# Optimization experiments

Hardware: AMD Instinct MI355X
Metric: run time of the kernel (lower is better)

The kernel has to match this reference:

```python
import jax, jax.numpy as jnp
import numpy as np

N_SPARSE = 26
VOCAB = 50000
EMB_DIM = 64
DENSE_DIM = 13
INPUT_DIM = N_SPARSE * EMB_DIM + DENSE_DIM  # 1677
HIDDEN = [1024, 512, 256]
N_CROSS = 3
BATCH = 16384
EPS = 1e-5


def setup_inputs() -> dict:
    key = jax.random.key(0)
    ks = jax.random.split(key, 24)
    inp = {}
    inp["sparse_data"] = jax.random.randint(ks[0], (BATCH, N_SPARSE), 0, VOCAB, dtype=jnp.int64 if jax.config.jax_enable_x64 else jnp.int32)
    inp["dense_data"] = jax.random.normal(ks[1], (BATCH, DENSE_DIM), dtype=jnp.float32)
    # stacked embedding tables [F, V, E] (nn.Embedding default init N(0,1); scaled down for stability)
    inp["emb_tables"] = jax.random.normal(ks[2], (N_SPARSE, VOCAB, EMB_DIM), dtype=jnp.float32) * 0.1
    # cross layers: Linear(input_dim, 1) per layer -> weight [L, D], bias [L]
    inp["w_cross"] = jax.random.normal(ks[3], (N_CROSS, INPUT_DIM), dtype=jnp.float32) * 0.02
    inp["b_cross"] = jnp.zeros((N_CROSS,), dtype=jnp.float32)
    # deep tower
    inp["bn0_g"] = jnp.ones((INPUT_DIM,), jnp.float32); inp["bn0_b"] = jnp.zeros((INPUT_DIM,), jnp.float32)
    inp["W1"] = jax.random.normal(ks[4], (INPUT_DIM, HIDDEN[0]), jnp.float32) * 0.02
    inp["bias1"] = jnp.zeros((HIDDEN[0],), jnp.float32)
    inp["bn1_g"] = jnp.ones((HIDDEN[0],), jnp.float32); inp["bn1_b"] = jnp.zeros((HIDDEN[0],), jnp.float32)
    inp["W2"] = jax.random.normal(ks[5], (HIDDEN[0], HIDDEN[1]), jnp.float32) * 0.02
    inp["bias2"] = jnp.zeros((HIDDEN[1],), jnp.float32)
    inp["bn2_g"] = jnp.ones((HIDDEN[1],), jnp.float32); inp["bn2_b"] = jnp.zeros((HIDDEN[1],), jnp.float32)
    inp["W3"] = jax.random.normal(ks[6], (HIDDEN[1], HIDDEN[2]), jnp.float32) * 0.02
    inp["bias3"] = jnp.zeros((HIDDEN[2],), jnp.float32)
    inp["bn3_g"] = jnp.ones((HIDDEN[2],), jnp.float32); inp["bn3_b"] = jnp.zeros((HIDDEN[2],), jnp.float32)
    # predict: Linear(hidden[-1] + input_dim, 1)
    inp["Wp"] = jax.random.normal(ks[7], (HIDDEN[2] + INPUT_DIM, 1), jnp.float32) * 0.02
    inp["bp"] = jnp.zeros((1,), jnp.float32)
    return inp


def _bn(x, g, b):
    # BatchNorm1d, training mode: biased batch stats over batch dim
    mu = jnp.mean(x, axis=0)
    var = jnp.mean((x - mu) ** 2, axis=0)
    return g * (x - mu) * jax.lax.rsqrt(var + EPS) + b


def reference(sparse_data, dense_data, emb_tables, w_cross, b_cross,
              bn0_g, bn0_b, W1, bias1, bn1_g, bn1_b, W2, bias2, bn2_g, bn2_b,
              W3, bias3, bn3_g, bn3_b, Wp, bp):
    # --- embedding (faithful to source bug: column 0 is used for every feature) ---
    idx0 = sparse_data[:, 0]                         # [B]
    emb = emb_tables[:, idx0, :]                     # [F, B, E]
    emb = jnp.transpose(emb, (1, 0, 2)).reshape(idx0.shape[0], -1)  # [B, F*E]

    x0 = jnp.concatenate([emb, dense_data], axis=1)  # [B, D]

    # --- cross network: Linear_i(x0^T x0) + x0 == x0*(x0@w_i) + b_i + x0 ---
    # (source restarts from cross_input each iteration, so only last layer matters;
    #  loop kept for fidelity, it is cheap)
    cross = x0
    for i in range(N_CROSS):
        s = x0 @ w_cross[i]                          # [B]
        cross = x0 * s[:, None] + b_cross[i] + x0    # [B, D]

    # --- deep tower: BN -> (Linear -> Dropout(eval=id) -> BN) x3, no activations ---
    h = _bn(x0, bn0_g, bn0_b)
    h = _bn(h @ W1 + bias1, bn1_g, bn1_b)
    h = _bn(h @ W2 + bias2, bn2_g, bn2_b)
    h = _bn(h @ W3 + bias3, bn3_g, bn3_b)

    out = jnp.concatenate([cross, h], axis=1) @ Wp + bp  # [B, 1]
    return jax.nn.sigmoid(out)
```

## Files before the change

### kernel.cpp

```cpp
#include <hip/hip_runtime.h>
#include <hip/hip_bf16.h>
#include <cstdint>
#include <cstddef>

#define AS1 __attribute__((address_space(1)))
#define AS3 __attribute__((address_space(3)))

typedef __attribute__((ext_vector_type(8))) short short8v;
typedef __attribute__((ext_vector_type(4))) float f32x4;
typedef unsigned short u16;

constexpr int kBatch = 16384;
constexpr int kNSp   = 26;
constexpr int kVocab = 50000;
constexpr int kEmb   = 64;
constexpr int kInDim = 1677;
constexpr int kInPad = 1728;
constexpr int kDense = 13;
constexpr int kH1 = 1024, kH2 = 512, kH3 = 256;
constexpr float kEps = 1e-5f;

constexpr int kStatsFloats = 2 * (kInPad + kH1 + kH2 + kH3);
constexpr int kBfFloats    = kH1 + kH2 + kH3;

__device__ __forceinline__ float b2f(u16 s) {
  unsigned u = ((unsigned)s) << 16;
  union { unsigned u; float f; } c; c.u = u; return c.f;
}
__device__ __forceinline__ u16 f2b(float f) {
  __hip_bfloat16 h = __float2bfloat16(f);
  return __builtin_bit_cast(u16, h);
}

__global__ void gather_kernel(const int* __restrict__ sparse, const float* __restrict__ dense,
                              const float* __restrict__ emb, const float* __restrict__ w_cross,
                              const float* __restrict__ b_cross, const float* __restrict__ Wp,
                              u16* __restrict__ x0, float* __restrict__ crossc,
                              float* __restrict__ stats) {
  const int b = blockIdx.x;
  const int tid = threadIdx.x;
  if (b == 0) {
    for (int i = tid; i < kStatsFloats + kBfFloats; i += 256) stats[i] = 0.f;
  }
  const int idx = sparse[b * kNSp];
  const float* wc2 = w_cross + 2 * kInDim;
  u16* xrow = x0 + (size_t)b * kInPad;
  float u = 0.f, v = 0.f, w = 0.f;
  for (int q = tid; q < 416; q += 256) {
    int p = q * 4;
    const float* src = emb + ((size_t)(p >> 6) * kVocab + idx) * kEmb + (p & 63);
    float4 val = *(const float4*)src;
    float4 wp  = *(const float4*)(Wp + p);
    u += val.x * wc2[p] + val.y * wc2[p + 1] + val.z * wc2[p + 2] + val.w * wc2[p + 3];
    v += val.x * wp.x + val.y * wp.y + val.z * wp.z + val.w * wp.w;
    w += wp.x + wp.y + wp.z + wp.w;
    ushort4 o;
    o.x = f2b(val.x); o.y = f2b(val.y); o.z = f2b(val.z); o.w = f2b(val.w);
    *(ushort4*)(xrow + p) = o;
  }
  int p = 1664 + tid;
  if (p < kInPad) {
    float val = 0.f;
    if (p < kInDim) {
      val = dense[b * kDense + (p - 1664)];
      float wp = Wp[p];
      u += val * wc2[p];
      v += val * wp;
      w += wp;
    }
    xrow[p] = f2b(val);
  }
  #pragma unroll
  for (int off = 32; off; off >>= 1) {
    u += __shfl_down(u, off, 64);
    v += __shfl_down(v, off, 64);
    w += __shfl_down(w, off, 64);
  }
  __shared__ float su[4], sv[4], sw[4];
  int lane = tid & 63, wv = tid >> 6;
  if (lane == 0) { su[wv] = u; sv[wv] = v; sw[wv] = w; }
  __syncthreads();
  if (tid == 0) {
    float uu = su[0] + su[1] + su[2] + su[3];
    float vv = sv[0] + sv[1] + sv[2] + sv[3];
    float ww = sw[0] + sw[1] + sw[2] + sw[3];
    crossc[b] = (1.f + uu) * vv + b_cross[2] * ww;
  }
}

__global__ __launch_bounds__(256) void colstats_kernel(
    const u16* __restrict__ X, int ld, float* __restrict__ sum, float* __restrict__ sq) {
  const int tid = threadIdx.x;
  const int cg = tid & 7;
  const int rg = tid >> 3;
  const int col0 = blockIdx.x * 64 + cg * 8;
  const int r0 = blockIdx.y * 512 + rg;
  float s[8] = {0,0,0,0,0,0,0,0}, s2[8] = {0,0,0,0,0,0,0,0};
  for (int i = 0; i < 16; ++i) {
    int r = r0 + i * 32;
    short8v v = *(const short8v*)(X + (size_t)r * ld + col0);
    #pragma unroll
    for (int e = 0; e < 8; ++e) {
      float f = b2f((u16)v[e]);
      s[e] += f; s2[e] += f * f;
    }
  }
  __shared__ float sh[256][17];
  #pragma unroll
  for (int e = 0; e < 8; ++e) { sh[tid][e] = s[e]; sh[tid][e + 8] = s2[e]; }
  __syncthreads();
  if (tid < 64) {
    int cgr = tid >> 3, e = tid & 7;
    float ts = 0.f, tq = 0.f;
    #pragma unroll
    for (int g = 0; g < 32; ++g) {
      ts += sh[g * 8 + cgr][e];
      tq += sh[g * 8 + cgr][e + 8];
    }
    int col = blockIdx.x * 64 + cgr * 8 + e;
    atomicAdd(&sum[col], ts);
    atomicAdd(&sq[col],  tq);
  }
}

__global__ void fold_kernel(const float* __restrict__ W, const float* __restrict__ sum,
                            const float* __restrict__ sq, const float* __restrict__ g,
                            const float* __restrict__ bb, float invM,
                            u16* __restrict__ Wt, float* __restrict__ bfold,
                            int K, int N, int Kp) {
  __shared__ float t[64][65];
  int kb = blockIdx.x * 64;
  int nb = blockIdx.y * 64;
  int c  = threadIdx.x & 63;
  int r0 = threadIdx.x >> 6;
  #pragma unroll
  for (int rr = 0; rr < 64; rr += 4) {
    int k = kb + rr + r0;
    t[rr + r0][c] = (k < K) ? W[(size_t)k * N + nb + c] : 0.f;
  }
  __syncthreads();
  int k = kb + c;
  float a = 0.f, cc = 0.f;
  if (k < K) {
    float mu  = sum[k] * invM;
    float var = sq[k] * invM - mu * mu;
    a  = g[k] * rsqrtf(var + kEps);
    cc = bb[k] - a * mu;
  }
  #pragma unroll
  for (int rr = 0; rr < 64; rr += 4) {
    int n = nb + rr + r0;
    float w = t[c][rr + r0];
    Wt[(size_t)n * Kp + k] = f2b(w * a);
    float part = cc * w;
    #pragma unroll
    for (int off = 32; off; off >>= 1) part += __shfl_xor(part, off, 64);
    if (c == 0) atomicAdd(&bfold[n], part);
  }
}

__global__ __launch_bounds__(256) void gemm_kernel(
    const u16* __restrict__ A, const u16* __restrict__ Bt,
    const float* __restrict__ bias, const float* __restrict__ bfold,
    u16* __restrict__ Z, float* __restrict__ sum, float* __restrict__ sq,
    int M, int N, int Kp) {
  __shared__ char lds[32768];
  char* ldsA = lds;
  char* ldsB = lds + 16384;
  const int tid  = threadIdx.x;
  const int lane = tid & 63;
  const int wv   = tid >> 6;
  const int wr = wv >> 1, wc = wv & 1;
  const int r16 = lane & 15, kg = lane >> 4;

  const int L   = blockIdx.y * gridDim.x + blockIdx.x;
  const int xcd = L & 7;
  const int j   = L >> 3;
  const int mb  = xcd * 16 + (j & 15);
  const int nb  = j >> 4;
  const int m0 = mb * 128;
  const int n0 = nb * 128;
  const int ldb = Kp * 2;

  const char* gA = (const char*)A + (size_t)m0 * ldb;
  const char* gB = (const char*)Bt + (size_t)n0 * ldb;

  const char* srcA[4]; const char* srcB[4]; int dst[4];
  #pragma unroll
  for (int rr = 0; rr < 4; ++rr) {
    int lb  = (rr * 256 + tid) * 16;
    int row = lb >> 7;
    int kb  = lb & 127;
    int kbs = kb ^ ((row & 7) << 4);
    dst[rr]  = lb;
    srcA[rr] = gA + (size_t)row * ldb + kbs;
    srcB[rr] = gB + (size_t)row * ldb + kbs;
  }

  f32x4 acc[4][4];
  #pragma unroll
  for (int m = 0; m < 4; ++m)
    #pragma unroll
    for (int n = 0; n < 4; ++n) acc[m][n] = (f32x4){0.f, 0.f, 0.f, 0.f};

  for (int k0 = 0; k0 < Kp; k0 += 64) {
    __syncthreads();
    #pragma unroll
    for (int rr = 0; rr < 4; ++rr)
      __builtin_amdgcn_global_load_lds((const AS1 unsigned*)(srcA[rr] + k0 * 2),
                                       (AS3 unsigned*)(ldsA + dst[rr]), 16, 0, 0);
    #pragma unroll
    for (int rr = 0; rr < 4; ++rr)
      __builtin_amdgcn_global_load_lds((const AS1 unsigned*)(srcB[rr] + k0 * 2),
                                       (AS3 unsigned*)(ldsB + dst[rr]), 16, 0, 0);
    asm volatile("s_waitcnt vmcnt(0)" ::: "memory");
    __syncthreads();
    #pragma unroll
    for (int kk = 0; kk < 2; ++kk) {
      short8v av[4], bv[4];
      #pragma unroll
      for (int m = 0; m < 4; ++m) {
        int row = wr * 64 + m * 16 + r16;
        int kb  = (kk * 64 + kg * 16) ^ ((row & 7) << 4);
        av[m] = *(const short8v*)(ldsA + row * 128 + kb);
      }
      #pragma unroll
      for (int n = 0; n < 4; ++n) {
        int row = wc * 64 + n * 16 + r16;
        int kb  = (kk * 64 + kg * 16) ^ ((row & 7) << 4);
        bv[n] = *(const short8v*)(ldsB + row * 128 + kb);
      }
      #pragma unroll
      for (int m = 0; m < 4; ++m)
        #pragma unroll
        for (int n = 0; n < 4; ++n)
          acc[m][n] = __builtin_amdgcn_mfma_f32_16x16x32_bf16(av[m], bv[n], acc[m][n], 0, 0, 0);
    }
  }
  #pragma unroll
  for (int n = 0; n < 4; ++n) {
    int col = n0 + wc * 64 + n * 16 + r16;
    float bs = bias[col] + bfold[col];
    float ps = 0.f, pq = 0.f;
    #pragma unroll
    for (int m = 0; m < 4; ++m) {
      int rbase = m0 + wr * 64 + m * 16 + kg * 4;
      #pragma unroll
      for (int j2 = 0; j2 < 4; ++j2) {
        float val = acc[m][n][j2] + bs;
        Z[(size_t)(rbase + j2) * N + col] = f2b(val);
        ps += val; pq += val * val;
      }
    }
    ps += __shfl_xor(ps, 16, 64); ps += __shfl_xor(ps, 32, 64);
    pq += __shfl_xor(pq, 16, 64); pq += __shfl_xor(pq, 32, 64);
    if (lane < 16) {
      atomicAdd(&sum[col], ps);
      atomicAdd(&sq[col],  pq);
    }
  }
}

#define BAR_VMN(N)                                                              \
  {                                                                             \
    asm volatile("s_waitcnt vmcnt(" #N ")" ::: "memory");                       \
    __builtin_amdgcn_sched_barrier(0);                                          \
    __builtin_amdgcn_s_barrier();                                               \
    __builtin_amdgcn_sched_barrier(0);                                          \
  }
#define BAR_NOVM()                                                              \
  {                                                                             \
    __builtin_amdgcn_sched_barrier(0);                                          \
    __builtin_amdgcn_s_barrier();                                               \
    __builtin_amdgcn_sched_barrier(0);                                          \
  }

#define STAGE(OP, H, TILE)                                                      \
  {                                                                             \
    const char* sb = ((OP) ? gB : gA) + (size_t)((H) * 128) * ldb               \
                     + (size_t)(TILE) * 128 + srcoff;                           \
    char* db = lds + (((TILE) & 1) << 16) + ((OP) << 15) + ((H) << 14) + tid * 16; \
    __builtin_amdgcn_global_load_lds((const AS1 unsigned*)sb,                   \
                                     (AS3 unsigned*)db, 16, 0, 0);              \
    __builtin_amdgcn_global_load_lds((const AS1 unsigned*)(sb + 64 * (size_t)ldb), \
                                     (AS3 unsigned*)(db + 8192), 16, 0, 0);     \
  }

#define PHASE(T, MH, NH)                                                        \
  {                                                                             \
    char* la  = lds + (((T) & 1) << 16);                                        \
    char* lbp = la + 32768;                                                     \
    short8v av[4][2], bv[2][2];                                                 \
    _Pragma("unroll")                                                           \
    for (int fm = 0; fm < 4; ++fm) {                                            \
      int row = (MH) * 128 + wr * 64 + fm * 16 + r16;                           \
      _Pragma("unroll")                                                         \
      for (int kk = 0; kk < 2; ++kk) {                                          \
        int kb = (kk * 64 + kg * 16) ^ ((row & 7) << 4);                        \
        av[fm][kk] = *(const short8v*)(la + row * 128 + kb);                    \
      }                                                                         \
    }                                                                           \
    _Pragma("unroll")                                                           \
    for (int fn = 0; fn < 2; ++fn) {                                            \
      int row = (NH) * 128 + wc * 32 + fn * 16 + r16;                           \
      _Pragma("unroll")                                                         \
      for (int kk = 0; kk < 2; ++kk) {                                          \
        int kb = (kk * 64 + kg * 16) ^ ((row & 7) << 4);                        \
        bv[fn][kk] = *(const short8v*)(lbp + row * 128 + kb);                   \
      }                                                                         \
    }                                                                           \
    __builtin_amdgcn_s_setprio(1);                                              \
    _Pragma("unroll")                                                           \
    for (int fm = 0; fm < 4; ++fm)                                              \
      _Pragma("unroll")                                                         \
      for (int fn = 0; fn < 2; ++fn)                                            \
        _Pragma("unroll")                                                       \
        for (int kk = 0; kk < 2; ++kk)                                          \
          acc[(MH) * 4 + fm][(NH) * 2 + fn] =                                   \
              __builtin_amdgcn_mfma_f32_16x16x32_bf16(                          \
                  av[fm][kk], bv[fn][kk],                                       \
                  acc[(MH) * 4 + fm][(NH) * 2 + fn], 0, 0, 0);                  \
    __builtin_amdgcn_s_setprio(0);                                              \
  }

__global__ __launch_bounds__(512, 2) void gemm256_kernel(
    const u16* __restrict__ A, const u16* __restrict__ Bt,
    const float* __restrict__ bias, const float* __restrict__ bfold,
    u16* __restrict__ Z, float* __restrict__ sum, float* __restrict__ sq,
    int M, int N, int Kp) {
  __shared__ char lds[131072];
  const int tid  = threadIdx.x;
  const int lane = tid & 63;
  const int wid  = tid >> 6;
  const int wr = wid >> 2, wc = wid & 3;
  const int r16 = lane & 15, kg = lane >> 4;

  const int nmb = M >> 8;
  const int cpx = nmb >> 3;
  const int L   = blockIdx.x;
  const int xcd = L & 7;
  const int jj  = L >> 3;
  const int mb  = xcd * cpx + (jj % cpx);
  const int nb  = jj / cpx;
  const int m0  = mb * 256;
  const int n0  = nb * 256;
  const int ldb = Kp * 2;
  const int nt  = Kp >> 6;

  const char* gA = (const char*)A + (size_t)m0 * ldb;
  const char* gB = (const char*)Bt + (size_t)n0 * ldb;
  const int row0 = tid >> 3;
  const int kbs  = ((tid & 7) * 16) ^ ((row0 & 7) << 4);
  const size_t srcoff = (size_t)row0 * ldb + kbs;

  f32x4 acc[8][4];
  #pragma unroll
  for (int m = 0; m < 8; ++m)
    #pragma unroll
    for (int n = 0; n < 4; ++n) acc[m][n] = (f32x4){0.f, 0.f, 0.f, 0.f};

  STAGE(0, 0, 0); STAGE(1, 0, 0); STAGE(1, 1, 0); STAGE(0, 1, 0);
  STAGE(0, 0, 1); STAGE(1, 0, 1);
  BAR_VMN(8);

  const int Tmain = nt - 2;
  for (int T = 0; T < Tmain; ++T) {
    STAGE(1, 1, T + 1);
    PHASE(T, 0, 0);
    BAR_VMN(8);
    STAGE(0, 1, T + 1);
    PHASE(T, 0, 1);
    BAR_VMN(8);
    if (T + 2 < nt) STAGE(0, 0, T + 2);
    PHASE(T, 1, 0);
    BAR_NOVM();
    if (T + 2 < nt) STAGE(1, 0, T + 2);
    PHASE(T, 1, 1);
    BAR_VMN(8);
  }
  for (int T = Tmain; T < nt; ++T) {
    if (T + 1 < nt) STAGE(1, 1, T + 1);
    PHASE(T, 0, 0);
    BAR_VMN(0);
    if (T + 1 < nt) STAGE(0, 1, T + 1);
    PHASE(T, 0, 1);
    BAR_VMN(0);
    PHASE(T, 1, 0);
    BAR_NOVM();
    PHASE(T, 1, 1);
    BAR_VMN(0);
  }

  #pragma unroll
  for (int nh = 0; nh < 2; ++nh)
    #pragma unroll
    for (int fn = 0; fn < 2; ++fn) {
      int col = n0 + nh * 128 + wc * 32 + fn * 16 + r16;
      float bs = bias[col] + bfold[col];
      float ps = 0.f, pq = 0.f;
      #pragma unroll
      for (int mh = 0; mh < 2; ++mh)
        #pragma unroll
        for (int fm = 0; fm < 4; ++fm) {
          int rbase = m0 + mh * 128 + wr * 64 + fm * 16 + kg * 4;
          #pragma unroll
          for (int j2 = 0; j2 < 4; ++j2) {
            float val = acc[mh * 4 + fm][nh * 2 + fn][j2] + bs;
            Z[(size_t)(rbase + j2) * N + col] = f2b(val);
            ps += val; pq += val * val;
          }
        }
      ps += __shfl_xor(ps, 16, 64); ps += __shfl_xor(ps, 32, 64);
      pq += __shfl_xor(pq, 16, 64); pq += __shfl_xor(pq, 32, 64);
      if (lane < 16) {
        atomicAdd(&sum[col], ps);
        atomicAdd(&sq[col],  pq);
      }
    }
}

#define STAGE2A(H, TILE)                                                        \
  {                                                                             \
    const char* sb = gA + (size_t)((H) * 128) * ldb + (size_t)(TILE) * 128 + srcoff; \
    char* db = lds + (((TILE) & 1) << 15) + ((H) << 14) + tid * 16;             \
    __builtin_amdgcn_global_load_lds((const AS1 unsigned*)sb,                   \
                                     (AS3 unsigned*)db, 16, 0, 0);              \
    __builtin_amdgcn_global_load_lds((const AS1 unsigned*)(sb + 64 * (size_t)ldb), \
                                     (AS3 unsigned*)(db + 8192), 16, 0, 0);     \
  }
#define STAGE2B(TILE)                                                           \
  {                                                                             \
    const char* sb = gB + (size_t)(TILE) * 128 + srcoff;                        \
    char* db = lds + 65536 + (((TILE) & 1) << 14) + tid * 16;                   \
    __builtin_amdgcn_global_load_lds((const AS1 unsigned*)sb,                   \
                                     (AS3 unsigned*)db, 16, 0, 0);              \
    __builtin_amdgcn_global_load_lds((const AS1 unsigned*)(sb + 64 * (size_t)ldb), \
                                     (AS3 unsigned*)(db + 8192), 16, 0, 0);     \
  }

#define PHASE2(T, MH)                                                           \
  {                                                                             \
    char* la  = lds + (((T) & 1) << 15) + ((MH) << 14);                         \
    char* lbp = lds + 65536 + (((T) & 1) << 14);                                \
    short8v av[4][2], bv[2][2];                                                 \
    _Pragma("unroll")                                                           \
    for (int fm = 0; fm < 4; ++fm) {                                            \
      int row = wr * 64 + fm * 16 + r16;                                        \
      _Pragma("unroll")                                                         \
      for (int kk = 0; kk < 2; ++kk) {                                          \
        int kb = (kk * 64 + kg * 16) ^ ((row & 7) << 4);                        \
        av[fm][kk] = *(const short8v*)(la + row * 128 + kb);                    \
      }                                                                         \
    }                                                                           \
    _Pragma("unroll")                                                           \
    for (int fn = 0; fn < 2; ++fn) {                                            \
      int row = wc * 32 + fn * 16 + r16;                                        \
      _Pragma("unroll")                                                         \
      for (int kk = 0; kk < 2; ++kk) {                                          \
        int kb = (kk * 64 + kg * 16) ^ ((row & 7) << 4);                        \
        bv[fn][kk] = *(const short8v*)(lbp + row * 128 + kb);                   \
      }                                                                         \
    }                                                                           \
    __builtin_amdgcn_s_setprio(1);                                              \
    _Pragma("unroll")                                                           \
    for (int fm = 0; fm < 4; ++fm)                                              \
      _Pragma("unroll")                                                         \
      for (int fn = 0; fn < 2; ++fn)                                            \
        _Pragma("unroll")                                                       \
        for (int kk = 0; kk < 2; ++kk)                                          \
          acc[(MH) * 4 + fm][fn] =                                              \
              __builtin_amdgcn_mfma_f32_16x16x32_bf16(                          \
                  av[fm][kk], bv[fn][kk], acc[(MH) * 4 + fm][fn], 0, 0, 0);     \
    __builtin_amdgcn_s_setprio(0);                                              \
  }

__global__ __launch_bounds__(512, 2) void gemm256x128_kernel(
    const u16* __restrict__ A, const u16* __restrict__ Bt,
    const float* __restrict__ bias, const float* __restrict__ bfold,
    u16* __restrict__ Z, float* __restrict__ sum, float* __restrict__ sq,
    int M, int N, int Kp) {
  __shared__ char lds[98304];
  const int tid  = threadIdx.x;
  const int lane = tid & 63;
  const int wid  = tid >> 6;
  const int wr = wid >> 2, wc = wid & 3;
  const int r16 = lane & 15, kg = lane >> 4;

  const int nmb = M >> 8;
  const int cpx = nmb >> 3;
  const int L   = blockIdx.x;
  const int xcd = L & 7;
  const int jj  = L >> 3;
  const int mb  = xcd * cpx + (jj % cpx);
  const int nb  = jj / cpx;
  const int m0  = mb * 256;
  const int n0  = nb * 128;
  const int ldb = Kp * 2;
  const int nt  = Kp >> 6;

  const char* gA = (const char*)A + (size_t)m0 * ldb;
  const char* gB = (const char*)Bt + (size_t)n0 * ldb;
  const int row0 = tid >> 3;
  const int kbs  = ((tid & 7) * 16) ^ ((row0 & 7) << 4);
  const size_t srcoff = (size_t)row0 * ldb + kbs;

  f32x4 acc[8][2];
  #pragma unroll
  for (int m = 0; m < 8; ++m)
    #pragma unroll
    for (int n = 0; n < 2; ++n) acc[m][n] = (f32x4){0.f, 0.f, 0.f, 0.f};

  STAGE2A(0, 0); STAGE2B(0); STAGE2A(1, 0);

  const int Tmain = nt - 1;
  for (int T = 0; T < Tmain; ++T) {
    STAGE2A(0, T + 1); STAGE2B(T + 1);
    BAR_VMN(6);
    PHASE2(T, 0);
    STAGE2A(1, T + 1);
    BAR_VMN(6);
    PHASE2(T, 1);
    BAR_NOVM();
  }
  BAR_VMN(2);
  PHASE2(nt - 1, 0);
  BAR_VMN(0);
  PHASE2(nt - 1, 1);

  #pragma unroll
  for (int fn = 0; fn < 2; ++fn) {
    int col = n0 + wc * 32 + fn * 16 + r16;
    float bs = bias[col] + bfold[col];
    float ps = 0.f, pq = 0.f;
    #pragma unroll
    for (int mh = 0; mh < 2; ++mh)
      #pragma unroll
      for (int fm = 0; fm < 4; ++fm) {
        int rbase = m0 + mh * 128 + wr * 64 + fm * 16 + kg * 4;
        #pragma unroll
        for (int j2 = 0; j2 < 4; ++j2) {
          float val = acc[mh * 4 + fm][fn][j2] + bs;
          Z[(size_t)(rbase + j2) * N + col] = f2b(val);
          ps += val; pq += val * val;
        }
      }
    ps += __shfl_xor(ps, 16, 64); ps += __shfl_xor(ps, 32, 64);
    pq += __shfl_xor(pq, 16, 64); pq += __shfl_xor(pq, 32, 64);
    if (lane < 16) {
      atomicAdd(&sum[col], ps);
      atomicAdd(&sq[col],  pq);
    }
  }
}

__global__ void final_kernel(const u16* __restrict__ z3, const float* __restrict__ sum3,
                             const float* __restrict__ sq3, const float* __restrict__ g3,
                             const float* __restrict__ b3, float invM,
                             const float* __restrict__ Wp, const float* __restrict__ bp,
                             const float* __restrict__ crossc, float* __restrict__ out) {
  int wv = threadIdx.x >> 6, lane = threadIdx.x & 63;
  int b = blockIdx.x * 4 + wv;
  const float* wph = Wp + kInDim;
  float s = 0.f;
  #pragma unroll
  for (int k = lane; k < kH3; k += 64) {
    float mu  = sum3[k] * invM;
    float var = sq3[k] * invM - mu * mu;
    float a   = g3[k] * rsqrtf(var + kEps);
    float cc  = b3[k] - a * mu;
    float h = a * b2f(z3[(size_t)b * kH3 + k]) + cc;
    s += h * wph[k];
  }
  #pragma unroll
  for (int off = 32; off; off >>= 1) s += __shfl_down(s, off, 64);
  if (lane == 0) {
    float logit = s + crossc[b] + bp[0];
    out[b] = 1.f / (1.f + expf(-logit));
  }
}

constexpr size_t OFF_X0    = 0;
constexpr size_t OFF_Z1    = OFF_X0 + (size_t)kBatch * kInPad * 2;
constexpr size_t OFF_Z2    = OFF_Z1 + (size_t)kBatch * kH1 * 2;
constexpr size_t OFF_Z3    = OFF_Z2 + (size_t)kBatch * kH2 * 2;
constexpr size_t OFF_W1T   = OFF_Z3 + (size_t)kBatch * kH3 * 2;
constexpr size_t OFF_W2T   = OFF_W1T + (size_t)kH1 * kInPad * 2;
constexpr size_t OFF_W3T   = OFF_W2T + (size_t)kH2 * kH1 * 2;
constexpr size_t OFF_CROSS = OFF_W3T + (size_t)kH3 * kH2 * 2;
constexpr size_t OFF_STATS = OFF_CROSS + (size_t)kBatch * 4;
constexpr size_t OFF_BF    = OFF_STATS + (size_t)kStatsFloats * 4;

extern "C" void kernel_launch(void* const* d_in, const int* in_sizes, int n_in,
                              void* d_out, int out_size, void* d_ws, size_t ws_size,
                              hipStream_t stream) {
  const int*   sparse  = (const int*)d_in[0];
  const float* dense   = (const float*)d_in[1];
  const float* emb     = (const float*)d_in[2];
  const float* w_cross = (const float*)d_in[3];
  const float* b_cross = (const float*)d_in[4];
  const float* bn0_g = (const float*)d_in[5],  *bn0_b = (const float*)d_in[6];
  const float* W1    = (const float*)d_in[7],  *bias1 = (const float*)d_in[8];
  const float* bn1_g = (const float*)d_in[9],  *bn1_b = (const float*)d_in[10];
  const float* W2    = (const float*)d_in[11], *bias2 = (const float*)d_in[12];
  const float* bn2_g = (const float*)d_in[13], *bn2_b = (const float*)d_in[14];
  const float* W3    = (const float*)d_in[15], *bias3 = (const float*)d_in[16];
  const float* bn3_g = (const float*)d_in[17], *bn3_b = (const float*)d_in[18];
  const float* Wp    = (const float*)d_in[19], *bp    = (const float*)d_in[20];

  char* ws = (char*)d_ws;
  u16* x0  = (u16*)(ws + OFF_X0);
  u16* z1  = (u16*)(ws + OFF_Z1);
  u16* z2  = (u16*)(ws + OFF_Z2);
  u16* z3  = (u16*)(ws + OFF_Z3);
  u16* W1t = (u16*)(ws + OFF_W1T);
  u16* W2t = (u16*)(ws + OFF_W2T);
  u16* W3t = (u16*)(ws + OFF_W3T);
  float* crossc = (float*)(ws + OFF_CROSS);
  float* stats  = (float*)(ws + OFF_STATS);
  float* sum0 = stats,            *sq0 = stats + kInPad;
  float* sum1 = sq0 + kInPad,     *sq1 = sum1 + kH1;
  float* sum2 = sq1 + kH1,        *sq2 = sum2 + kH2;
  float* sum3 = sq2 + kH2,        *sq3 = sum3 + kH3;
  float* bfold = (float*)(ws + OFF_BF);
  float* b1f = bfold, *b2f = b1f + kH1, *b3f = b2f + kH2;
  float* out = (float*)d_out;

  const float invM = 1.f / (float)kBatch;

  gather_kernel<<<kBatch, 256, 0, stream>>>(sparse, dense, emb, w_cross, b_cross, Wp,
                                            x0, crossc, stats);

  colstats_kernel<<<dim3(kInPad / 64, kBatch / 512), 256, 0, stream>>>(x0, kInPad, sum0, sq0);
  fold_kernel<<<dim3(kInPad / 64, kH1 / 64), 256, 0, stream>>>(
      W1, sum0, sq0, bn0_g, bn0_b, invM, W1t, b1f, kInDim, kH1, kInPad);

  gemm256_kernel<<<(kBatch / 256) * (kH1 / 256), 512, 0, stream>>>(
      x0, W1t, bias1, b1f, z1, sum1, sq1, kBatch, kH1, kInPad);
  fold_kernel<<<dim3(kH1 / 64, kH2 / 64), 256, 0, stream>>>(
      W2, sum1, sq1, bn1_g, bn1_b, invM, W2t, b2f, kH1, kH2, kH1);

  gemm256x128_kernel<<<(kBatch / 256) * (kH2 / 128), 512, 0, stream>>>(
      z1, W2t, bias2, b2f, z2, sum2, sq2, kBatch, kH2, kH1);
  fold_kernel<<<dim3(kH2 / 64, kH3 / 64), 256, 0, stream>>>(
      W3, sum2, sq2, bn2_g, bn2_b, invM, W3t, b3f, kH2, kH3, kH2);

  gemm_kernel<<<dim3(kH3 / 128, kBatch / 128), 256, 0, stream>>>(
      z2, W3t, bias3, b3f, z3, sum3, sq3, kBatch, kH3, kH2);

  final_kernel<<<kBatch / 4, 256, 0, stream>>>(z3, sum3, sq3, bn3_g, bn3_b, invM,
                                               Wp, bp, crossc, out);
}
```

Measured before the change: 197.8 us.

## Double-buffer LDS in gemm_kernel to overlap global loads with MFMA

The 128x128 gemm_kernel moves from a single LDS buffer, where it waited for all loads before computing each K-tile, to two LDS buffers. The next tile is prefetched with global_load_lds while the current tile feeds the MFMAs, and the wait becomes vmcnt(8) instead of vmcnt(0). It also raises wave priority around the MFMA block. The cost is doubled LDS use (64KB), which may lower occupancy, and the gain is limited to whichever GEMMs use this kernel rather than the other pipelined kernel.

```diff
diff --git a/kernel.cpp b/kernel.cpp
--- a/kernel.cpp
+++ b/kernel.cpp
@@ -159,14 +159,26 @@
   }
 }
 
+#define BAR_VMN(N)                                                              \
+  {                                                                             \
+    asm volatile("s_waitcnt vmcnt(" #N ")" ::: "memory");                       \
+    __builtin_amdgcn_sched_barrier(0);                                          \
+    __builtin_amdgcn_s_barrier();                                               \
+    __builtin_amdgcn_sched_barrier(0);                                          \
+  }
+#define BAR_NOVM()                                                              \
+  {                                                                             \
+    __builtin_amdgcn_sched_barrier(0);                                          \
+    __builtin_amdgcn_s_barrier();                                               \
+    __builtin_amdgcn_sched_barrier(0);                                          \
+  }
+
 __global__ __launch_bounds__(256) void gemm_kernel(
     const u16* __restrict__ A, const u16* __restrict__ Bt,
     const float* __restrict__ bias, const float* __restrict__ bfold,
     u16* __restrict__ Z, float* __restrict__ sum, float* __restrict__ sq,
     int M, int N, int Kp) {
-  __shared__ char lds[32768];
-  char* ldsA = lds;
-  char* ldsB = lds + 16384;
+  __shared__ char lds[65536];
   const int tid  = threadIdx.x;
   const int lane = tid & 63;
   const int wv   = tid >> 6;
@@ -181,6 +193,7 @@
   const int m0 = mb * 128;
   const int n0 = nb * 128;
   const int ldb = Kp * 2;
+  const int nt  = Kp >> 6;
 
   const char* gA = (const char*)A + (size_t)m0 * ldb;
   const char* gB = (const char*)Bt + (size_t)n0 * ldb;
@@ -197,46 +210,65 @@
     srcB[rr] = gB + (size_t)row * ldb + kbs;
   }
 
+#define STAGE3(TILE)                                                            \
+  {                                                                             \
+    char* la = lds + (((TILE) & 1) << 14);                                      \
+    char* lb = lds + 32768 + (((TILE) & 1) << 14);                              \
+    _Pragma("unroll")                                                           \
+    for (int rr = 0; rr < 4; ++rr)                                              \
+      __builtin_amdgcn_global_load_lds((const AS1 unsigned*)(srcA[rr] + (size_t)(TILE) * 128), \
+                                       (AS3 unsigned*)(la + dst[rr]), 16, 0, 0); \
+    _Pragma("unroll")                                                           \
+    for (int rr = 0; rr < 4; ++rr)                                              \
+      __builtin_amdgcn_global_load_lds((const AS1 unsigned*)(srcB[rr] + (size_t)(TILE) * 128), \
+                                       (AS3 unsigned*)(lb + dst[rr]), 16, 0, 0); \
+  }
+
   f32x4 acc[4][4];
   #pragma unroll
   for (int m = 0; m < 4; ++m)
     #pragma unroll
     for (int n = 0; n < 4; ++n) acc[m][n] = (f32x4){0.f, 0.f, 0.f, 0.f};
 
-  for (int k0 = 0; k0 < Kp; k0 += 64) {
-    __syncthreads();
-    #pragma unroll
-    for (int rr = 0; rr < 4; ++rr)
-      __builtin_amdgcn_global_load_lds((const AS1 unsigned*)(srcA[rr] + k0 * 2),
-                                       (AS3 unsigned*)(ldsA + dst[rr]), 16, 0, 0);
-    #pragma unroll
-    for (int rr = 0; rr < 4; ++rr)
-      __builtin_amdgcn_global_load_lds((const AS1 unsigned*)(srcB[rr] + k0 * 2),
-                                       (AS3 unsigned*)(ldsB + dst[rr]), 16, 0, 0);
-    asm volatile("s_waitcnt vmcnt(0)" ::: "memory");
-    __syncthreads();
-    #pragma unroll
-    for (int kk = 0; kk < 2; ++kk) {
-      short8v av[4], bv[4];
+  STAGE3(0);
+  for (int T = 0; T < nt; ++T) {
+    if (T + 1 < nt) {
+      STAGE3(T + 1);
+      BAR_VMN(8);
+    } else {
+      BAR_VMN(0);
+    }
+    {
+      char* la  = lds + ((T & 1) << 14);
+      char* lbp = lds + 32768 + ((T & 1) << 14);
       #pragma unroll
-      for (int m = 0; m < 4; ++m) {
-        int row = wr * 64 + m * 16 + r16;
-        int kb  = (kk * 64 + kg * 16) ^ ((row & 7) << 4);
-        av[m] = *(const short8v*)(ldsA + row * 128 + kb);
+      for (int kk = 0; kk < 2; ++kk) {
+        short8v av[4], bv[4];
+        #pragma unroll
+        for (int m = 0; m < 4; ++m) {
+          int row = wr * 64 + m * 16 + r16;
+          int kb  = (kk * 64 + kg * 16) ^ ((row & 7) << 4);
+          av[m] = *(const short8v*)(la + row * 128 + kb);
+        }
+        #pragma unroll
+        for (int n = 0; n < 4; ++n) {
+          int row = wc * 64 + n * 16 + r16;
+          int kb  = (kk * 64 + kg * 16) ^ ((row & 7) << 4);
+          bv[n] = *(const short8v*)(lbp + row * 128 + kb);
+        }
+        __builtin_amdgcn_s_setprio(1);
+        #pragma unroll
+        for (int m = 0; m < 4; ++m)
+          #pragma unroll
+          for (int n = 0; n < 4; ++n)
+            acc[m][n] = __builtin_amdgcn_mfma_f32_16x16x32_bf16(av[m], bv[n], acc[m][n], 0, 0, 0);
+        __builtin_amdgcn_s_setprio(0);
       }
-      #pragma unroll
-      for (int n = 0; n < 4; ++n) {
-        int row = wc * 64 + n * 16 + r16;
-        int kb  = (kk * 64 + kg * 16) ^ ((row & 7) << 4);
-        bv[n] = *(const short8v*)(ldsB + row * 128 + kb);
-      }
-      #pragma unroll
-      for (int m = 0; m < 4; ++m)
-        #pragma unroll
-        for (int n = 0; n < 4; ++n)
-          acc[m][n] = __builtin_amdgcn_mfma_f32_16x16x32_bf16(av[m], bv[n], acc[m][n], 0, 0, 0);
-    }
-  }
+    }
+    BAR_NOVM();
+  }
+#undef STAGE3
+
   #pragma unroll
   for (int n = 0; n < 4; ++n) {
     int col = n0 + wc * 64 + n * 16 + r16;
@@ -260,20 +292,6 @@
     }
   }
 }
-
-#define BAR_VMN(N)                                                              \
-  {                                                                             \
-    asm volatile("s_waitcnt vmcnt(" #N ")" ::: "memory");                       \
-    __builtin_amdgcn_sched_barrier(0);                                          \
-    __builtin_amdgcn_s_barrier();                                               \
-    __builtin_amdgcn_sched_barrier(0);                                          \
-  }
-#define BAR_NOVM()                                                              \
-  {                                                                             \
-    __builtin_amdgcn_sched_barrier(0);                                          \
-    __builtin_amdgcn_s_barrier();                                               \
-    __builtin_amdgcn_sched_barrier(0);                                          \
-  }
 
 #define STAGE(OP, H, TILE)                                                      \
   {                                                                             \
```

Result: faster. 192.7 us (-2.6%).
